# Optimization experiments

Hardware: AMD Instinct MI355X
Metric: run time of the kernel (lower is better)

## Reference

```python
import jax, jax.numpy as jnp
import numpy as np
from jax import lax

DN = ('NCHW', 'OIHW', 'NCHW')

def _conv(x, w, pad):
    return lax.conv_general_dilated(x, w, (1, 1), [(pad, pad), (pad, pad)], dimension_numbers=DN)

def _bn(x, g, b, eps=1e-5):
    # BatchNorm2d in training mode: batch statistics over (N,H,W), biased variance
    m = jnp.mean(x, axis=(0, 2, 3), keepdims=True)
    v = jnp.var(x, axis=(0, 2, 3), keepdims=True)
    return (x - m) * lax.rsqrt(v + eps) * g.reshape(1, -1, 1, 1) + b.reshape(1, -1, 1, 1)

def setup_inputs() -> dict:
    key = jax.random.key(0)
    ks = jax.random.split(key, 24)
    B, H, W = 128, 64, 64
    l_i, lh = 2, (150, 120, 100)
    l_q, cf = 10, H * W
    r = lambda k, s, sc: jax.random.normal(k, s, dtype=jnp.float32) * sc
    return {
        'X': r(ks[0], (B, l_i, H, W), 1.0),
        'obs': r(ks[1], (B, 24), 1.0),
        'h1_w': r(ks[2], (lh[0], l_i, 3, 3), 0.1), 'h1_b': r(ks[3], (lh[0],), 0.05),
        'g1': jnp.ones((lh[0],), jnp.float32), 'b1': jnp.zeros((lh[0],), jnp.float32),
        'h2_w': r(ks[4], (lh[1], lh[0], 3, 3), 0.03), 'h2_b': r(ks[5], (lh[1],), 0.05),
        'g2': jnp.ones((lh[1],), jnp.float32), 'b2': jnp.zeros((lh[1],), jnp.float32),
        'h3_w': r(ks[6], (lh[2], lh[1], 3, 3), 0.03), 'h3_b': r(ks[7], (lh[2],), 0.05),
        'g3': jnp.ones((lh[2],), jnp.float32), 'b3': jnp.zeros((lh[2],), jnp.float32),
        'r_w': r(ks[8], (1, lh[2], 1, 1), 0.1),
        'q_w': r(ks[9], (l_q, 1, 5, 5), 0.1),
        'w': r(ks[10], (l_q, 1, 5, 5), 0.05),  # Parameter (zeros init in torch; randn here for nontrivial math)
        'fc1_w': r(ks[11], (100, 24), 0.1), 'fc1_b': r(ks[12], (100,), 0.05),
        'fc2_w': r(ks[13], (10, 100), 0.1), 'fc2_b': r(ks[14], (10,), 0.05),
        'cv_w': r(ks[15], (1, cf), 0.02), 'cv_b': r(ks[16], (1,), 0.05),
        'K': 36,
    }

def reference(X, obs, h1_w, h1_b, g1, b1, h2_w, h2_b, g2, b2, h3_w, h3_b, g3, b3,
              r_w, q_w, w, fc1_w, fc1_b, fc2_w, fc2_b, cv_w, cv_b, K):
    relu = jax.nn.relu
    h = relu(_bn(_conv(X, h1_w, 1) + h1_b.reshape(1, -1, 1, 1), g1, b1))
    h = relu(_bn(_conv(h, h2_w, 1) + h2_b.reshape(1, -1, 1, 1), g2, b2))
    h = relu(_bn(_conv(h, h3_w, 1) + h3_b.reshape(1, -1, 1, 1), g3, b3))
    r = _conv(h, r_w, 0)                      # [B,1,H,W] reward map
    qr = _conv(r, q_w, 2)                     # conv of r part is constant across VI iterations
    v = jnp.max(qr, axis=1, keepdims=True)    # [B,1,H,W]
    # conv2d(cat([r,v],1), cat([q_w,w],1)) == conv(r,q_w) + conv(v,w)
    def step(v, _):
        q = qr + _conv(v, w, 2)
        return jnp.max(q, axis=1, keepdims=True), None
    # original: K-1 loop iterations + 1 extra conv/max = K total steps after the init
    v, _ = lax.scan(step, v, None, length=K)
    critic = v.reshape(v.shape[0], -1) @ cv_w.T + cv_b
    action_pred = relu(relu(obs @ fc1_w.T + fc1_b) @ fc2_w.T + fc2_b)
    return (critic, action_pred)
```

## Files before the change

### kernel.cpp

```cpp
#include <hip/hip_runtime.h>


#define NHW 524288.0f

typedef __attribute__((ext_vector_type(8))) short v8s;
typedef __attribute__((ext_vector_type(4))) float v4f;

static __device__ __forceinline__ float bf2f(unsigned short u) {
  return __uint_as_float(((unsigned int)u) << 16);
}
static __device__ __forceinline__ unsigned short f2bf(float f) {
  unsigned int x = __float_as_uint(f);
  return (unsigned short)((x + 0x7fffu + ((x >> 16) & 1u)) >> 16);
}
static __device__ __forceinline__ float wave_sum(float s) {
  #pragma unroll
  for (int off = 32; off > 0; off >>= 1) s += __shfl_down(s, off, 64);
  return s;
}

template <int CO, int CI, int CIP>
__global__ __launch_bounds__(256) void repack_w(
    const float* __restrict__ w, unsigned short* __restrict__ Wp)
{
  int i = blockIdx.x * 256 + threadIdx.x;
  const int total = 9 * 128 * CIP;
  if (i >= total) return;
  int pos = i / (128 * CIP);
  int rem = i - pos * (128 * CIP);
  int co  = rem / CIP;
  int ci  = rem - co * CIP;
  float v = (co < CO && ci < CI) ? w[(co * CI + ci) * 9 + pos] : 0.f;
  Wp[i] = f2bf(v);
}

__global__ __launch_bounds__(256) void conv1_stats(
    const float* __restrict__ X, const float* __restrict__ w1,
    const float* __restrict__ b1, float* __restrict__ S, float* __restrict__ Q)
{
  const int tile = blockIdx.x;
  const int b    = tile >> 3;
  const int y0t  = (tile & 7) * 8;
  const int co0  = blockIdx.y * 15;
  const int tid  = threadIdx.x;
  const int x    = tid & 63;
  const int ly0  = (tid >> 6) * 2;

  __shared__ float lin[2][10][66];
  __shared__ float ss[15], qq[15];
  if (tid < 15) { ss[tid] = 0.f; qq[tid] = 0.f; }
  for (int idx = tid; idx < 2 * 10 * 66; idx += 256) {
    int cc = idx / 660, rem = idx - cc * 660;
    int rr = rem / 66,  c   = rem - rr * 66;
    int yy = y0t + rr - 1, xx = c - 1;
    lin[cc][rr][c] = (yy >= 0 && yy < 64 && xx >= 0 && xx < 64)
                         ? X[((size_t)(b * 2 + cc) << 12) + (yy << 6) + xx] : 0.f;
  }
  __syncthreads();

  float iv[2][4][3];
  #pragma unroll
  for (int cc = 0; cc < 2; cc++)
    #pragma unroll
    for (int r = 0; r < 4; r++)
      #pragma unroll
      for (int c = 0; c < 3; c++) iv[cc][r][c] = lin[cc][ly0 + r][x + c];

  #pragma unroll
  for (int co = 0; co < 15; co++) {
    const float* w9 = w1 + (size_t)(co0 + co) * 18;
    float a0 = 0.f, a1 = 0.f;
    #pragma unroll
    for (int cc = 0; cc < 2; cc++)
      #pragma unroll
      for (int ky = 0; ky < 3; ky++)
        #pragma unroll
        for (int kx = 0; kx < 3; kx++) {
          float wv = w9[cc * 9 + ky * 3 + kx];
          a0 = fmaf(iv[cc][ky][kx],     wv, a0);
          a1 = fmaf(iv[cc][ky + 1][kx], wv, a1);
        }
    float bz = b1[co0 + co];
    float t0 = a0 + bz, t1 = a1 + bz;
    float s  = wave_sum(t0 + t1);
    float q  = wave_sum(t0 * t0 + t1 * t1);
    if ((tid & 63) == 0) { atomicAdd(&ss[co], s); atomicAdd(&qq[co], q); }
  }
  __syncthreads();
  if (tid < 15) {
    atomicAdd(&S[co0 + tid], ss[tid]);
    atomicAdd(&Q[co0 + tid], qq[tid]);
  }
}

template <int C>
__global__ void bn_finalize(const float* __restrict__ S, const float* __restrict__ Q,
                            const float* __restrict__ g, const float* __restrict__ be,
                            float* __restrict__ A, float* __restrict__ Bs)
{
  int c = threadIdx.x;
  if (c < C) {
    const float invN = 1.f / NHW;
    float m   = S[c] * invN;
    float var = fmaxf(Q[c] * invN - m * m, 0.f);
    float sc  = g[c] * rsqrtf(var + 1e-5f);
    A[c]  = sc;
    Bs[c] = be[c] - m * sc;
  }
}

__global__ __launch_bounds__(256, 2) void conv2_mfma(
    const float* __restrict__ X,  const float* __restrict__ w1,
    const float* __restrict__ b1f, const float* __restrict__ A1,
    const float* __restrict__ B1, const unsigned short* __restrict__ W2p,
    const float* __restrict__ b2, unsigned short* __restrict__ t2,
    float* __restrict__ S2, float* __restrict__ Q2)
{
  const int bx   = blockIdx.x;
  const int b    = bx >> 4;
  const int t16  = bx & 15;
  const int y0   = (t16 >> 2) * 16;
  const int x0   = (t16 & 3) * 16;
  const int tid  = threadIdx.x;
  const int lane = tid & 63;
  const int wid  = __builtin_amdgcn_readfirstlane(tid >> 6);
  const int ln   = lane & 15;
  const int quad = (lane >> 4) * 8;

  __shared__ __align__(16) float Xs[2][20][20];
  __shared__ float w1s[2700];
  __shared__ float A1s[150], B1s[150], b1s[150], b2s[128];
  __shared__ float ssB[128], qqB[128];
  __shared__ __align__(16) unsigned short Atile[324 * 34];
  __shared__ __align__(16) unsigned short outs[256 * 68];

  for (int i = tid; i < 2700; i += 256) w1s[i] = w1[i];
  for (int i = tid; i < 150; i += 256) { A1s[i] = A1[i]; B1s[i] = B1[i]; b1s[i] = b1f[i]; }
  if (tid < 128) { b2s[tid] = (tid < 120) ? b2[tid] : 0.f; ssB[tid] = 0.f; qqB[tid] = 0.f; }
  for (int i = tid; i < 800; i += 256) {
    int c2 = i / 400, rem = i - c2 * 400;
    int rr = rem / 20, cc = rem - rr * 20;
    int gy = y0 - 2 + rr, gx = x0 - 2 + cc;
    Xs[c2][rr][cc] = (gy >= 0 && gy < 64 && gx >= 0 && gx < 64)
                         ? X[((size_t)(b * 2 + c2) << 12) + (gy << 6) + gx] : 0.f;
  }

  v4f acc[4][8];
  #pragma unroll
  for (int i = 0; i < 4; i++)
    #pragma unroll
    for (int j = 0; j < 8; j++) acc[i][j] = (v4f){0.f, 0.f, 0.f, 0.f};

  for (int chunk = 0; chunk < 5; chunk++) {
    __syncthreads();
    {
      const int ci_loc = tid & 31;
      const int ci = chunk * 32 + ci_loc;
      const bool live = (ci < 150);
      float wv[18], sc = 0.f, sh = 0.f, bz = 0.f;
      if (live) {
        #pragma unroll
        for (int k = 0; k < 18; k++) wv[k] = w1s[ci * 18 + k];
        sc = A1s[ci]; sh = B1s[ci]; bz = b1s[ci];
      }
      for (int pass = 0; pass < 41; pass++) {
        int p = pass * 8 + (tid >> 5);
        if (p < 324) {
          float v = 0.f;
          if (live) {
            int pr = p / 18, pc = p - pr * 18;
            int hy = y0 - 1 + pr, hx = x0 - 1 + pc;
            if (hy >= 0 && hy < 64 && hx >= 0 && hx < 64) {
              float a = bz;
              #pragma unroll
              for (int c2 = 0; c2 < 2; c2++)
                #pragma unroll
                for (int ky = 0; ky < 3; ky++)
                  #pragma unroll
                  for (int kx = 0; kx < 3; kx++)
                    a = fmaf(Xs[c2][pr + ky][pc + kx], wv[c2 * 9 + ky * 3 + kx], a);
              v = fmaxf(fmaf(a, sc, sh), 0.f);
            }
          }
          Atile[p * 34 + ci_loc] = f2bf(v);
        }
      }
    }
    __syncthreads();

    v8s afr[6][3];
    #pragma unroll
    for (int t = 0; t < 6; t++)
      #pragma unroll
      for (int kx = 0; kx < 3; kx++)
        afr[t][kx] = *(const v8s*)(&Atile[((wid * 4 + t) * 18 + ln + kx) * 34 + quad]);

    #pragma unroll
    for (int pos = 0; pos < 9; pos++) {
      const int ky = pos / 3, kx = pos - ky * 3;
      const unsigned short* bw =
          W2p + (size_t)(pos * 128 + ln) * 160 + chunk * 32 + quad;
      v8s bf[8];
      #pragma unroll
      for (int nj = 0; nj < 8; nj++)
        bf[nj] = *(const v8s*)(bw + (size_t)nj * 16 * 160);
      #pragma unroll
      for (int mi = 0; mi < 4; mi++) {
        #pragma unroll
        for (int nj = 0; nj < 8; nj++)
          acc[mi][nj] = __builtin_amdgcn_mfma_f32_16x16x32_bf16(
              afr[mi + ky][kx], bf[nj], acc[mi][nj], 0, 0, 0);
      }
    }
  }

  #pragma unroll
  for (int half = 0; half < 2; half++) {
    __syncthreads();
    #pragma unroll
    for (int mi = 0; mi < 4; mi++)
      #pragma unroll
      for (int njl = 0; njl < 4; njl++) {
        int n = njl * 16 + ln;
        float bz = b2s[half * 64 + n];
        #pragma unroll
        for (int r2 = 0; r2 < 4; r2++) {
          int m = wid * 64 + mi * 16 + (lane >> 4) * 4 + r2;
          outs[m * 68 + n] = f2bf(acc[mi][half * 4 + njl][r2] + bz);
        }
      }
    __syncthreads();
    const int ng = half ? 7 : 8;
    for (int i = tid; i < 256 * ng; i += 256) {
      int p = i / ng, g = i - p * ng;
      int gy = y0 + (p >> 4), gx = x0 + (p & 15);
      size_t gpx = ((size_t)b << 12) + (gy << 6) + gx;
      *(uint4*)(t2 + gpx * 120 + half * 64 + g * 8) =
          *(const uint4*)(&outs[p * 68 + g * 8]);
    }
    {
      float ls = 0.f, lq = 0.f;
      const int c = tid & 63, pr0 = (tid >> 6) * 64;
      for (int p = 0; p < 64; p++) {
        float v = bf2f(outs[(pr0 + p) * 68 + c]);
        ls += v; lq += v * v;
      }
      atomicAdd(&ssB[half * 64 + c], ls);
      atomicAdd(&qqB[half * 64 + c], lq);
    }
  }
  __syncthreads();
  if (tid < 120) {
    atomicAdd(&S2[tid], ssB[tid]);
    atomicAdd(&Q2[tid], qqB[tid]);
  }
}

__global__ __launch_bounds__(256, 2) void conv3_mfma(
    const unsigned short* __restrict__ t2, const float* __restrict__ A2,
    const float* __restrict__ B2, const unsigned short* __restrict__ W3p,
    const float* __restrict__ b3, unsigned short* __restrict__ t3,
    float* __restrict__ S3, float* __restrict__ Q3)
{
  const int bx   = blockIdx.x;
  const int b    = bx >> 4;
  const int t16  = bx & 15;
  const int y0   = (t16 >> 2) * 16;
  const int x0   = (t16 & 3) * 16;
  const int tid  = threadIdx.x;
  const int lane = tid & 63;
  const int wid  = __builtin_amdgcn_readfirstlane(tid >> 6);
  const int ln   = lane & 15;
  const int quad = (lane >> 4) * 8;

  __shared__ float A2s[120], B2s[120], b3s[128];
  __shared__ float ssB[128], qqB[128];
  __shared__ __align__(16) unsigned short Atile[324 * 34];
  __shared__ __align__(16) unsigned short outs[256 * 68];

  for (int i = tid; i < 120; i += 256) { A2s[i] = A2[i]; B2s[i] = B2[i]; }
  if (tid < 128) { b3s[tid] = (tid < 100) ? b3[tid] : 0.f; ssB[tid] = 0.f; qqB[tid] = 0.f; }

  v4f acc[4][8];
  #pragma unroll
  for (int i = 0; i < 4; i++)
    #pragma unroll
    for (int j = 0; j < 8; j++) acc[i][j] = (v4f){0.f, 0.f, 0.f, 0.f};

  for (int chunk = 0; chunk < 4; chunk++) {
    __syncthreads();
    {
      const int ci0 = chunk * 32;
      const int ngr = (chunk == 3) ? 3 : 4;
      for (int i = tid; i < 1296; i += 256) {
        int p = i >> 2, g = i & 3;
        int pr = p / 18, pc = p - pr * 18;
        int hy = y0 - 1 + pr, hx = x0 - 1 + pc;
        union { uint4 v; unsigned short u[8]; } ov;
        ov.v = (uint4){0, 0, 0, 0};
        if (g < ngr && hy >= 0 && hy < 64 && hx >= 0 && hx < 64) {
          size_t gpx = ((size_t)b << 12) + (hy << 6) + hx;
          union { uint4 v; unsigned short u[8]; } in;
          in.v = *(const uint4*)(t2 + gpx * 120 + ci0 + g * 8);
          #pragma unroll
          for (int j = 0; j < 8; j++) {
            int ci = ci0 + g * 8 + j;
            ov.u[j] = f2bf(fmaxf(fmaf(bf2f(in.u[j]), A2s[ci], B2s[ci]), 0.f));
          }
        }
        *(uint4*)(&Atile[p * 34 + g * 8]) = ov.v;
      }
    }
    __syncthreads();

    v8s afr[6][3];
    #pragma unroll
    for (int t = 0; t < 6; t++)
      #pragma unroll
      for (int kx = 0; kx < 3; kx++)
        afr[t][kx] = *(const v8s*)(&Atile[((wid * 4 + t) * 18 + ln + kx) * 34 + quad]);

    #pragma unroll
    for (int pos = 0; pos < 9; pos++) {
      const int ky = pos / 3, kx = pos - ky * 3;
      const unsigned short* bw =
          W3p + (size_t)(pos * 128 + ln) * 128 + chunk * 32 + quad;
      v8s bf[8];
      #pragma unroll
      for (int nj = 0; nj < 8; nj++)
        bf[nj] = *(const v8s*)(bw + (size_t)nj * 16 * 128);
      #pragma unroll
      for (int mi = 0; mi < 4; mi++) {
        #pragma unroll
        for (int nj = 0; nj < 8; nj++)
          acc[mi][nj] = __builtin_amdgcn_mfma_f32_16x16x32_bf16(
              afr[mi + ky][kx], bf[nj], acc[mi][nj], 0, 0, 0);
      }
    }
  }

  #pragma unroll
  for (int half = 0; half < 2; half++) {
    __syncthreads();
    #pragma unroll
    for (int mi = 0; mi < 4; mi++)
      #pragma unroll
      for (int njl = 0; njl < 4; njl++) {
        int n = njl * 16 + ln;
        float bz = b3s[half * 64 + n];
        #pragma unroll
        for (int r2 = 0; r2 < 4; r2++) {
          int m = wid * 64 + mi * 16 + (lane >> 4) * 4 + r2;
          outs[m * 68 + n] = f2bf(acc[mi][half * 4 + njl][r2] + bz);
        }
      }
    __syncthreads();
    const int ng = half ? 5 : 8;
    for (int i = tid; i < 256 * ng; i += 256) {
      int p = i / ng, g = i - p * ng;
      int gy = y0 + (p >> 4), gx = x0 + (p & 15);
      size_t gpx = ((size_t)b << 12) + (gy << 6) + gx;
      *(uint4*)(t3 + gpx * 104 + half * 64 + g * 8) =
          *(const uint4*)(&outs[p * 68 + g * 8]);
    }
    {
      float ls = 0.f, lq = 0.f;
      const int c = tid & 63, pr0 = (tid >> 6) * 64;
      for (int p = 0; p < 64; p++) {
        float v = bf2f(outs[(pr0 + p) * 68 + c]);
        ls += v; lq += v * v;
      }
      atomicAdd(&ssB[half * 64 + c], ls);
      atomicAdd(&qqB[half * 64 + c], lq);
    }
  }
  __syncthreads();
  if (tid < 100) {
    atomicAdd(&S3[tid], ssB[tid]);
    atomicAdd(&Q3[tid], qqB[tid]);
  }
}

__global__ __launch_bounds__(256) void bn3_reduce_r(
    const unsigned short* __restrict__ t3, const float* __restrict__ A3,
    const float* __restrict__ B3, const float* __restrict__ rw,
    float* __restrict__ r)
{
  __shared__ float A3s[104], B3s[104], rws[104];
  const int tid = threadIdx.x;
  for (int i = tid; i < 104; i += 256) {
    bool v = (i < 100);
    A3s[i] = v ? A3[i] : 0.f;
    B3s[i] = v ? B3[i] : 0.f;
    rws[i] = v ? rw[i] : 0.f;
  }
  __syncthreads();

  size_t px = (size_t)blockIdx.x * 256 + tid;
  const unsigned short* p = t3 + px * 104;
  float a = 0.f;
  #pragma unroll
  for (int gq = 0; gq < 13; gq++) {
    union { uint4 v; unsigned short u[8]; } in;
    in.v = *(const uint4*)(p + gq * 8);
    #pragma unroll
    for (int j = 0; j < 8; j++) {
      int ci = gq * 8 + j;
      a = fmaf(fmaxf(fmaf(bf2f(in.u[j]), A3s[ci], B3s[ci]), 0.f), rws[ci], a);
    }
  }
  r[px] = a;
}

__global__ __launch_bounds__(256) void qr_init(
    const float* __restrict__ r, const float* __restrict__ qw,
    unsigned short* __restrict__ qr, float* __restrict__ v0)
{
  const int tile = blockIdx.x;
  const int b    = tile >> 4;
  const int y0t  = (tile & 15) * 4;
  const int tid  = threadIdx.x;
  const int x    = tid & 63;
  const int ly   = tid >> 6;

  __shared__ float lv[8][68];
  for (int idx = tid; idx < 8 * 68; idx += 256) {
    int rr = idx / 68, c = idx - rr * 68;
    int yy = y0t + rr - 2, xx = c - 2;
    lv[rr][c] = (yy >= 0 && yy < 64 && xx >= 0 && xx < 64)
                    ? r[((size_t)b << 12) + (yy << 6) + xx] : 0.f;
  }
  __syncthreads();

  float iv[5][5];
  #pragma unroll
  for (int ky = 0; ky < 5; ky++)
    #pragma unroll
    for (int kx = 0; kx < 5; kx++) iv[ky][kx] = lv[ly + ky][x + kx];

  const int y = y0t + ly;
  float vmax = -1e30f;
  #pragma unroll
  for (int a = 0; a < 10; a++) {
    float q = 0.f;
    #pragma unroll
    for (int ky = 0; ky < 5; ky++)
      #pragma unroll
      for (int kx = 0; kx < 5; kx++)
        q = fmaf(iv[ky][kx], qw[a * 25 + ky * 5 + kx], q);
    qr[((size_t)(b * 10 + a) << 12) + (y << 6) + x] = f2bf(q);
    vmax = fmaxf(vmax, q);
  }
  v0[((size_t)b << 12) + (y << 6) + x] = vmax;
}

__global__ __launch_bounds__(256) void vi_step(
    const float* __restrict__ vin, const unsigned short* __restrict__ qr,
    const float* __restrict__ ww, float* __restrict__ vout)
{
  const int tile = blockIdx.x;
  const int b    = tile >> 4;
  const int y0t  = (tile & 15) * 4;
  const int tid  = threadIdx.x;
  const int x    = tid & 63;
  const int ly   = tid >> 6;

  __shared__ float lv[8][68];
  for (int idx = tid; idx < 8 * 68; idx += 256) {
    int rr = idx / 68, c = idx - rr * 68;
    int yy = y0t + rr - 2, xx = c - 2;
    lv[rr][c] = (yy >= 0 && yy < 64 && xx >= 0 && xx < 64)
                    ? vin[((size_t)b << 12) + (yy << 6) + xx] : 0.f;
  }
  __syncthreads();

  float iv[5][5];
  #pragma unroll
  for (int ky = 0; ky < 5; ky++)
    #pragma unroll
    for (int kx = 0; kx < 5; kx++) iv[ky][kx] = lv[ly + ky][x + kx];

  const int y = y0t + ly;
  float vmax = -1e30f;
  #pragma unroll
  for (int a = 0; a < 10; a++) {
    float q = bf2f(qr[((size_t)(b * 10 + a) << 12) + (y << 6) + x]);
    #pragma unroll
    for (int ky = 0; ky < 5; ky++)
      #pragma unroll
      for (int kx = 0; kx < 5; kx++)
        q = fmaf(iv[ky][kx], ww[a * 25 + ky * 5 + kx], q);
    vmax = fmaxf(vmax, q);
  }
  vout[((size_t)b << 12) + (y << 6) + x] = vmax;
}

__global__ __launch_bounds__(256) void critic_k(
    const float* __restrict__ v, const float* __restrict__ cvw,
    const float* __restrict__ cvb, float* __restrict__ out)
{
  const int b = blockIdx.x;
  const int tid = threadIdx.x;
  const float4* pv = (const float4*)(v + ((size_t)b << 12));
  const float4* pw = (const float4*)cvw;
  float s = 0.f;
  #pragma unroll
  for (int i = 0; i < 4; i++) {
    float4 a = pv[tid + 256 * i];
    float4 w = pw[tid + 256 * i];
    s += a.x * w.x + a.y * w.y + a.z * w.z + a.w * w.w;
  }
  s = wave_sum(s);
  __shared__ float ls[4];
  const int w = tid >> 6;
  if ((tid & 63) == 0) ls[w] = s;
  __syncthreads();
  if (tid == 0) out[b] = ls[0] + ls[1] + ls[2] + ls[3] + cvb[0];
}

__global__ __launch_bounds__(128) void action_k(
    const float* __restrict__ obs, const float* __restrict__ fc1w,
    const float* __restrict__ fc1b, const float* __restrict__ fc2w,
    const float* __restrict__ fc2b, float* __restrict__ out)
{
  const int b = blockIdx.x;
  const int j = threadIdx.x;
  __shared__ float ob[24];
  __shared__ float h[100];
  if (j < 24) ob[j] = obs[b * 24 + j];
  __syncthreads();
  if (j < 100) {
    float s = fc1b[j];
    #pragma unroll
    for (int k = 0; k < 24; k++) s = fmaf(ob[k], fc1w[j * 24 + k], s);
    h[j] = fmaxf(s, 0.f);
  }
  __syncthreads();
  if (j < 10) {
    float s = fc2b[j];
    for (int k = 0; k < 100; k++) s = fmaf(h[k], fc2w[j * 100 + k], s);
    out[128 + b * 10 + j] = fmaxf(s, 0.f);
  }
}

extern "C" void kernel_launch(void* const* d_in, const int* in_sizes, int n_in,
                              void* d_out, int out_size, void* d_ws,
                              size_t ws_size, hipStream_t stream)
{
  const float* X     = (const float*)d_in[0];
  const float* obs   = (const float*)d_in[1];
  const float* h1_w  = (const float*)d_in[2];
  const float* h1_b  = (const float*)d_in[3];
  const float* g1    = (const float*)d_in[4];
  const float* b1    = (const float*)d_in[5];
  const float* h2_w  = (const float*)d_in[6];
  const float* h2_b  = (const float*)d_in[7];
  const float* g2    = (const float*)d_in[8];
  const float* b2    = (const float*)d_in[9];
  const float* h3_w  = (const float*)d_in[10];
  const float* h3_b  = (const float*)d_in[11];
  const float* g3    = (const float*)d_in[12];
  const float* b3    = (const float*)d_in[13];
  const float* r_w   = (const float*)d_in[14];
  const float* q_w   = (const float*)d_in[15];
  const float* w_vi  = (const float*)d_in[16];
  const float* fc1_w = (const float*)d_in[17];
  const float* fc1_b = (const float*)d_in[18];
  const float* fc2_w = (const float*)d_in[19];
  const float* fc2_b = (const float*)d_in[20];
  const float* cv_w  = (const float*)d_in[21];
  const float* cv_b  = (const float*)d_in[22];

  char* ws = (char*)d_ws;
  unsigned short* t2  = (unsigned short*)ws;
  unsigned short* t3  = (unsigned short*)(ws + 125829120ull);
  unsigned short* W2p = (unsigned short*)(ws + 234881024ull);
  unsigned short* W3p = (unsigned short*)(ws + 235249664ull);
  float*          ST  = (float*)         (ws + 235544576ull);
  float* S1 = ST +    0; float* Q1 = ST +  150; float* A1 = ST +  300; float* B1 = ST +  450;
  float* S2 = ST +  600; float* Q2 = ST +  720; float* A2 = ST +  840; float* B2 = ST +  960;
  float* S3 = ST + 1080; float* Q3 = ST + 1180; float* A3 = ST + 1280; float* B3 = ST + 1380;
  float*          r   = (float*)ws;
  unsigned short* qrh = (unsigned short*)(ws + 2097152ull);
  float*          vA  = (float*)(ws + 12582912ull);
  float*          vB  = (float*)(ws + 14680064ull);

  hipMemsetAsync(ST, 0, 1480 * sizeof(float), stream);

  repack_w<120, 150, 160><<<720, 256, 0, stream>>>(h2_w, W2p);
  repack_w<100, 120, 128><<<576, 256, 0, stream>>>(h3_w, W3p);

  conv1_stats<<<dim3(1024, 10), 256, 0, stream>>>(X, h1_w, h1_b, S1, Q1);
  bn_finalize<150><<<1, 256, 0, stream>>>(S1, Q1, g1, b1, A1, B1);

  conv2_mfma<<<2048, 256, 0, stream>>>(X, h1_w, h1_b, A1, B1, W2p, h2_b, t2, S2, Q2);
  bn_finalize<120><<<1, 256, 0, stream>>>(S2, Q2, g2, b2, A2, B2);

  conv3_mfma<<<2048, 256, 0, stream>>>(t2, A2, B2, W3p, h3_b, t3, S3, Q3);
  bn_finalize<100><<<1, 256, 0, stream>>>(S3, Q3, g3, b3, A3, B3);

  bn3_reduce_r<<<2048, 256, 0, stream>>>(t3, A3, B3, r_w, r);

  qr_init<<<2048, 256, 0, stream>>>(r, q_w, qrh, vA);
  for (int i = 0; i < 36; i++) {
    const float* vin = (i & 1) ? vB : vA;
    float* vout      = (i & 1) ? vA : vB;
    vi_step<<<2048, 256, 0, stream>>>(vin, qrh, w_vi, vout);
  }

  float* out = (float*)d_out;
  critic_k<<<128, 256, 0, stream>>>(vA, cv_w, cv_b, out);
  action_k<<<128, 128, 0, stream>>>(obs, fc1_w, fc1_b, fc2_w, fc2_b, out);
}
```

Before: 1.294 ms.

## Fuse pairs of VI steps, alias LDS buffers, fold BN stats into epilogue

Value-iteration steps are fused two per launch: each block computes an intermediate value map with a halo in shared memory and then the second step, halving the launch count at the cost of redundant halo computation. The conv2/conv3 kernels alias their input, tile and output staging buffers in one shared array to cut LDS use, and raise the occupancy hint to 3 blocks. BN sum and sum-of-squares are now accumulated from registers in the epilogue with shuffles, replacing a separate pass over LDS. Aliasing depends on barrier ordering, and the higher occupancy target may force register spills.

```diff
diff --git a/kernel.cpp b/kernel.cpp
--- a/kernel.cpp
+++ b/kernel.cpp
@@ -109,7 +109,7 @@
   }
 }
 
-__global__ __launch_bounds__(256, 2) void conv2_mfma(
+__global__ __launch_bounds__(256, 3) void conv2_mfma(
     const float* __restrict__ X,  const float* __restrict__ w1,
     const float* __restrict__ b1f, const float* __restrict__ A1,
     const float* __restrict__ B1, const unsigned short* __restrict__ W2p,
@@ -127,12 +127,15 @@
   const int ln   = lane & 15;
   const int quad = (lane >> 4) * 8;
 
-  __shared__ __align__(16) float Xs[2][20][20];
-  __shared__ float w1s[2700];
-  __shared__ float A1s[150], B1s[150], b1s[150], b2s[128];
-  __shared__ float ssB[128], qqB[128];
-  __shared__ __align__(16) unsigned short Atile[324 * 34];
-  __shared__ __align__(16) unsigned short outs[256 * 68];
+  __shared__ __align__(16) unsigned int U[9460];
+  float*          Xs    = (float*)U;
+  float*          w1s   = (float*)(U + 800);
+  float*          A1s   = (float*)(U + 3500);
+  float*          B1s   = (float*)(U + 3650);
+  float*          b1s   = (float*)(U + 3800);
+  unsigned short* Atile = (unsigned short*)(U + 3952);
+  unsigned short* outs  = (unsigned short*)U;
+  __shared__ float b2s[128], ssB[128], qqB[128];
 
   for (int i = tid; i < 2700; i += 256) w1s[i] = w1[i];
   for (int i = tid; i < 150; i += 256) { A1s[i] = A1[i]; B1s[i] = B1[i]; b1s[i] = b1f[i]; }
@@ -141,8 +144,8 @@
     int c2 = i / 400, rem = i - c2 * 400;
     int rr = rem / 20, cc = rem - rr * 20;
     int gy = y0 - 2 + rr, gx = x0 - 2 + cc;
-    Xs[c2][rr][cc] = (gy >= 0 && gy < 64 && gx >= 0 && gx < 64)
-                         ? X[((size_t)(b * 2 + c2) << 12) + (gy << 6) + gx] : 0.f;
+    Xs[i] = (gy >= 0 && gy < 64 && gx >= 0 && gx < 64)
+                ? X[((size_t)(b * 2 + c2) << 12) + (gy << 6) + gx] : 0.f;
   }
 
   v4f acc[4][8];
@@ -178,7 +181,8 @@
                 for (int ky = 0; ky < 3; ky++)
                   #pragma unroll
                   for (int kx = 0; kx < 3; kx++)
-                    a = fmaf(Xs[c2][pr + ky][pc + kx], wv[c2 * 9 + ky * 3 + kx], a);
+                    a = fmaf(Xs[c2 * 400 + (pr + ky) * 20 + (pc + kx)],
+                             wv[c2 * 9 + ky * 3 + kx], a);
               v = fmaxf(fmaf(a, sc, sh), 0.f);
             }
           }
@@ -218,17 +222,27 @@
   for (int half = 0; half < 2; half++) {
     __syncthreads();
     #pragma unroll
-    for (int mi = 0; mi < 4; mi++)
-      #pragma unroll
-      for (int njl = 0; njl < 4; njl++) {
-        int n = njl * 16 + ln;
-        float bz = b2s[half * 64 + n];
+    for (int njl = 0; njl < 4; njl++) {
+      int n = njl * 16 + ln;
+      float bz = b2s[half * 64 + n];
+      float ls = 0.f, lq = 0.f;
+      #pragma unroll
+      for (int mi = 0; mi < 4; mi++)
         #pragma unroll
         for (int r2 = 0; r2 < 4; r2++) {
           int m = wid * 64 + mi * 16 + (lane >> 4) * 4 + r2;
-          outs[m * 68 + n] = f2bf(acc[mi][half * 4 + njl][r2] + bz);
+          unsigned short us = f2bf(acc[mi][half * 4 + njl][r2] + bz);
+          outs[m * 68 + n] = us;
+          float v = bf2f(us);
+          ls += v; lq += v * v;
         }
-      }
+      ls += __shfl_xor(ls, 16); ls += __shfl_xor(ls, 32);
+      lq += __shfl_xor(lq, 16); lq += __shfl_xor(lq, 32);
+      if ((lane >> 4) == 0) {
+        atomicAdd(&ssB[half * 64 + n], ls);
+        atomicAdd(&qqB[half * 64 + n], lq);
+      }
+    }
     __syncthreads();
     const int ng = half ? 7 : 8;
     for (int i = tid; i < 256 * ng; i += 256) {
@@ -238,16 +252,6 @@
       *(uint4*)(t2 + gpx * 120 + half * 64 + g * 8) =
           *(const uint4*)(&outs[p * 68 + g * 8]);
     }
-    {
-      float ls = 0.f, lq = 0.f;
-      const int c = tid & 63, pr0 = (tid >> 6) * 64;
-      for (int p = 0; p < 64; p++) {
-        float v = bf2f(outs[(pr0 + p) * 68 + c]);
-        ls += v; lq += v * v;
-      }
-      atomicAdd(&ssB[half * 64 + c], ls);
-      atomicAdd(&qqB[half * 64 + c], lq);
-    }
   }
   __syncthreads();
   if (tid < 120) {
@@ -256,7 +260,7 @@
   }
 }
 
-__global__ __launch_bounds__(256, 2) void conv3_mfma(
+__global__ __launch_bounds__(256, 3) void conv3_mfma(
     const unsigned short* __restrict__ t2, const float* __restrict__ A2,
     const float* __restrict__ B2, const unsigned short* __restrict__ W3p,
     const float* __restrict__ b3, unsigned short* __restrict__ t3,
@@ -273,10 +277,11 @@
   const int ln   = lane & 15;
   const int quad = (lane >> 4) * 8;
 
-  __shared__ float A2s[120], B2s[120], b3s[128];
-  __shared__ float ssB[128], qqB[128];
-  __shared__ __align__(16) unsigned short Atile[324 * 34];
-  __shared__ __align__(16) unsigned short outs[256 * 68];
+  __shared__ __align__(16) unsigned int U[8704];
+  unsigned short* Atile = (unsigned short*)U;
+  unsigned short* outs  = (unsigned short*)U;
+  __shared__ float A2s[120], B2s[120];
+  __shared__ float b3s[128], ssB[128], qqB[128];
 
   for (int i = tid; i < 120; i += 256) { A2s[i] = A2[i]; B2s[i] = B2[i]; }
   if (tid < 128) { b3s[tid] = (tid < 100) ? b3[tid] : 0.f; ssB[tid] = 0.f; qqB[tid] = 0.f; }
@@ -343,17 +348,27 @@
   for (int half = 0; half < 2; half++) {
     __syncthreads();
     #pragma unroll
-    for (int mi = 0; mi < 4; mi++)
-      #pragma unroll
-      for (int njl = 0; njl < 4; njl++) {
-        int n = njl * 16 + ln;
-        float bz = b3s[half * 64 + n];
+    for (int njl = 0; njl < 4; njl++) {
+      int n = njl * 16 + ln;
+      float bz = b3s[half * 64 + n];
+      float ls = 0.f, lq = 0.f;
+      #pragma unroll
+      for (int mi = 0; mi < 4; mi++)
         #pragma unroll
         for (int r2 = 0; r2 < 4; r2++) {
           int m = wid * 64 + mi * 16 + (lane >> 4) * 4 + r2;
-          outs[m * 68 + n] = f2bf(acc[mi][half * 4 + njl][r2] + bz);
+          unsigned short us = f2bf(acc[mi][half * 4 + njl][r2] + bz);
+          outs[m * 68 + n] = us;
+          float v = bf2f(us);
+          ls += v; lq += v * v;
         }
-      }
+      ls += __shfl_xor(ls, 16); ls += __shfl_xor(ls, 32);
+      lq += __shfl_xor(lq, 16); lq += __shfl_xor(lq, 32);
+      if ((lane >> 4) == 0) {
+        atomicAdd(&ssB[half * 64 + n], ls);
+        atomicAdd(&qqB[half * 64 + n], lq);
+      }
+    }
     __syncthreads();
     const int ng = half ? 5 : 8;
     for (int i = tid; i < 256 * ng; i += 256) {
@@ -363,16 +378,6 @@
       *(uint4*)(t3 + gpx * 104 + half * 64 + g * 8) =
           *(const uint4*)(&outs[p * 68 + g * 8]);
     }
-    {
-      float ls = 0.f, lq = 0.f;
-      const int c = tid & 63, pr0 = (tid >> 6) * 64;
-      for (int p = 0; p < 64; p++) {
-        float v = bf2f(outs[(pr0 + p) * 68 + c]);
-        ls += v; lq += v * v;
-      }
-      atomicAdd(&ssB[half * 64 + c], ls);
-      atomicAdd(&qqB[half * 64 + c], lq);
-    }
   }
   __syncthreads();
   if (tid < 100) {
@@ -454,45 +459,67 @@
   v0[((size_t)b << 12) + (y << 6) + x] = vmax;
 }
 
-__global__ __launch_bounds__(256) void vi_step(
+__global__ __launch_bounds__(256) void vi_step2(
     const float* __restrict__ vin, const unsigned short* __restrict__ qr,
     const float* __restrict__ ww, float* __restrict__ vout)
 {
   const int tile = blockIdx.x;
-  const int b    = tile >> 4;
-  const int y0t  = (tile & 15) * 4;
+  const int b    = tile >> 2;
+  const int y0   = (tile & 3) * 16;
   const int tid  = threadIdx.x;
-  const int x    = tid & 63;
-  const int ly   = tid >> 6;
-
-  __shared__ float lv[8][68];
-  for (int idx = tid; idx < 8 * 68; idx += 256) {
-    int rr = idx / 68, c = idx - rr * 68;
-    int yy = y0t + rr - 2, xx = c - 2;
-    lv[rr][c] = (yy >= 0 && yy < 64 && xx >= 0 && xx < 64)
-                    ? vin[((size_t)b << 12) + (yy << 6) + xx] : 0.f;
-  }
-  __syncthreads();
-
-  float iv[5][5];
-  #pragma unroll
-  for (int ky = 0; ky < 5; ky++)
-    #pragma unroll
-    for (int kx = 0; kx < 5; kx++) iv[ky][kx] = lv[ly + ky][x + kx];
-
-  const int y = y0t + ly;
-  float vmax = -1e30f;
-  #pragma unroll
-  for (int a = 0; a < 10; a++) {
-    float q = bf2f(qr[((size_t)(b * 10 + a) << 12) + (y << 6) + x]);
-    #pragma unroll
-    for (int ky = 0; ky < 5; ky++)
-      #pragma unroll
-      for (int kx = 0; kx < 5; kx++)
-        q = fmaf(iv[ky][kx], ww[a * 25 + ky * 5 + kx], q);
-    vmax = fmaxf(vmax, q);
-  }
-  vout[((size_t)b << 12) + (y << 6) + x] = vmax;
+
+  __shared__ float lv[24][73];
+  __shared__ float mid[20][69];
+  __shared__ float wws[250];
+
+  for (int i = tid; i < 250; i += 256) wws[i] = ww[i];
+
+  for (int i = tid; i < 24 * 72; i += 256) {
+    int rr = i / 72, cc = i - rr * 72;
+    int yy = y0 - 4 + rr, xx = cc - 4;
+    lv[rr][cc] = (yy >= 0 && yy < 64 && xx >= 0 && xx < 64)
+                     ? vin[((size_t)b << 12) + (yy << 6) + xx] : 0.f;
+  }
+  __syncthreads();
+
+  for (int i = tid; i < 20 * 68; i += 256) {
+    int rr = i / 68, cc = i - rr * 68;
+    int yy = y0 - 2 + rr, xx = cc - 2;
+    float res = 0.f;
+    if (yy >= 0 && yy < 64 && xx >= 0 && xx < 64) {
+      float tap[25];
+      #pragma unroll
+      for (int t = 0; t < 25; t++) tap[t] = lv[rr + t / 5][cc + (t % 5)];
+      float vmax = -1e30f;
+      #pragma unroll
+      for (int a = 0; a < 10; a++) {
+        float q = bf2f(qr[((size_t)(b * 10 + a) << 12) + (yy << 6) + xx]);
+        #pragma unroll
+        for (int t = 0; t < 25; t++) q = fmaf(tap[t], wws[a * 25 + t], q);
+        vmax = fmaxf(vmax, q);
+      }
+      res = vmax;
+    }
+    mid[rr][cc] = res;
+  }
+  __syncthreads();
+
+  for (int i = tid; i < 16 * 64; i += 256) {
+    int rr = i >> 6, xx = i & 63;
+    int yy = y0 + rr;
+    float tap[25];
+    #pragma unroll
+    for (int t = 0; t < 25; t++) tap[t] = mid[rr + t / 5][xx + (t % 5)];
+    float vmax = -1e30f;
+    #pragma unroll
+    for (int a = 0; a < 10; a++) {
+      float q = bf2f(qr[((size_t)(b * 10 + a) << 12) + (yy << 6) + xx]);
+      #pragma unroll
+      for (int t = 0; t < 25; t++) q = fmaf(tap[t], wws[a * 25 + t], q);
+      vmax = fmaxf(vmax, q);
+    }
+    vout[((size_t)b << 12) + (yy << 6) + xx] = vmax;
+  }
 }
 
 __global__ __launch_bounds__(256) void critic_k(
@@ -602,10 +629,10 @@
   bn3_reduce_r<<<2048, 256, 0, stream>>>(t3, A3, B3, r_w, r);
 
   qr_init<<<2048, 256, 0, stream>>>(r, q_w, qrh, vA);
-  for (int i = 0; i < 36; i++) {
+  for (int i = 0; i < 18; i++) {
     const float* vin = (i & 1) ? vB : vA;
     float* vout      = (i & 1) ? vA : vB;
-    vi_step<<<2048, 256, 0, stream>>>(vin, qrh, w_vi, vout);
+    vi_step2<<<512, 256, 0, stream>>>(vin, qrh, w_vi, vout);
   }
 
   float* out = (float*)d_out;
```

Result: slower. 3.267 ms (+152.5%).
